# Optimization experiments

Measured on AMD Instinct MI355X. Metric: run time of the kernel, lower is better.

## Reference

```python
import jax, jax.numpy as jnp
import numpy as np

# B images, N objects/image, R relations/image; D=obj/rel feature dim, H=GGNN hidden,
# NO=num object classes, NR=num relation classes, T=GGNN time steps.
B, N, R, D, H, NO, NR, T = 8, 64, 2048, 4096, 512, 151, 51, 3


def setup_inputs() -> dict:
    key = jax.random.key(0)
    ks = jax.random.split(key, 24)
    nrm = lambda k, shp: jax.random.normal(k, shp, dtype=jnp.float32) * 0.02
    im_inds = jnp.repeat(jnp.arange(B, dtype=jnp.int32), N)          # sorted per-object image ids
    img_r = jnp.repeat(jnp.arange(B, dtype=jnp.int32), R)            # per-relation image ids
    pair = jax.random.randint(ks[0], (B * R, 2), 0, N, dtype=jnp.int32) + (img_r * N)[:, None]
    rel_inds = jnp.concatenate([img_r[:, None], pair], axis=1)        # [B*R, 3]
    return dict(
        im_inds=im_inds, rel_inds=rel_inds,
        obj_fmaps=jax.random.normal(ks[1], (B * N, D), jnp.float32),
        obj_logits=jax.random.normal(ks[2], (B * N, NO), jnp.float32),
        vr=jax.random.normal(ks[3], (B * R, D), jnp.float32),
        W_obj=nrm(ks[4], (D, H)), b_obj=jnp.zeros((H,), jnp.float32),
        W_rel=nrm(ks[5], (D, H)), b_rel=jnp.zeros((H,), jnp.float32),
        W_prob=nrm(ks[6], (NO, H)), b_prob=jnp.zeros((H,), jnp.float32),
        W_so=nrm(ks[7], (H, H)), W_oo=nrm(ks[8], (H, H)),
        W_rs=nrm(ks[9], (H, H)), W_ro=nrm(ks[10], (H, H)),
        Wz=nrm(ks[11], (H, H)), Uz=nrm(ks[12], (H, H)), bz=jnp.zeros((H,), jnp.float32),
        Wr=nrm(ks[13], (H, H)), Ur=nrm(ks[14], (H, H)), br=jnp.zeros((H,), jnp.float32),
        Wh=nrm(ks[15], (H, H)), Uh=nrm(ks[16], (H, H)), bh=jnp.zeros((H,), jnp.float32),
        W_out_rel=nrm(ks[17], (2 * H, H)), b_out_rel=jnp.zeros((H,), jnp.float32),
        W_cls_rel=nrm(ks[18], (H, NR)), b_cls_rel=jnp.zeros((NR,), jnp.float32),
        W_out_obj=nrm(ks[19], (2 * H, H)), b_out_obj=jnp.zeros((H,), jnp.float32),
        W_cls_obj=nrm(ks[20], (H, NO)), b_cls_obj=jnp.zeros((NO,), jnp.float32),
    )


def reference(im_inds, rel_inds, obj_fmaps, obj_logits, vr,
              W_obj, b_obj, W_rel, b_rel, W_prob, b_prob,
              W_so, W_oo, W_rs, W_ro,
              Wz, Uz, bz, Wr, Ur, br, Wh, Uh, bh,
              W_out_rel, b_out_rel, W_cls_rel, b_cls_rel,
              W_out_obj, b_out_obj, W_cls_obj, b_cls_obj):
    # obj_probs = softmax(obj_logits); project features + class distribution into GGNN hidden
    obj_probs = jax.nn.softmax(obj_logits, axis=-1)
    xo = (obj_fmaps @ W_obj + b_obj + obj_probs @ W_prob + b_prob).reshape(B, N, H)
    xr = (vr @ W_rel + b_rel).reshape(B, R, H)
    # per-image local indices: rel_inds[rel_s:rel_e, 1:] - obj_s
    off = (jnp.arange(B, dtype=rel_inds.dtype) * N)[:, None]
    subj = rel_inds[:, 1].reshape(B, R) - off
    objn = rel_inds[:, 2].reshape(B, R) - off

    def gru(h, m):
        z = jax.nn.sigmoid(m @ Wz + h @ Uz + bz)
        r = jax.nn.sigmoid(m @ Wr + h @ Ur + br)
        hh = jnp.tanh(m @ Wh + (r * h) @ Uh + bh)
        return (1.0 - z) * h + z * hh

    def per_image(xo_i, xr_i, s, o):
        ho, hr = xo_i, xr_i
        for _ in range(T):  # fixed recurrence depth (time_step_num)
            mr = ho[s] @ W_so + ho[o] @ W_oo                               # gather obj -> rel
            mo = (jax.ops.segment_sum(hr @ W_rs, s, num_segments=N)
                  + jax.ops.segment_sum(hr @ W_ro, o, num_segments=N))     # scatter rel -> obj
            ho, hr = gru(ho, mo), gru(hr, mr)
        rel_logits = jnp.tanh(jnp.concatenate([hr, xr_i], -1) @ W_out_rel + b_out_rel) @ W_cls_rel + b_cls_rel
        obj_ref = jnp.tanh(jnp.concatenate([ho, xo_i], -1) @ W_out_obj + b_out_obj) @ W_cls_obj + b_cls_obj
        return rel_logits, obj_ref

    rel_logits, obj_ref = jax.vmap(per_image)(xo, xr, subj, objn)
    rel_logits = rel_logits.reshape(B * R, NR)
    obj_ref = obj_ref.reshape(B * N, NO)
    scpred_softmax = jax.nn.softmax(rel_logits, axis=-1)
    scent_softmax = jax.nn.softmax(obj_ref, axis=-1)
    # sgcls, inference, no obj_labels: obj_preds = argmax over classes 1..NO-1, + 1
    obj_preds = jnp.argmax(obj_ref[:, 1:], axis=-1) + 1
    return (obj_ref, obj_preds, rel_logits, scpred_softmax, scent_softmax)
```

## Files before the change

kernel.cpp:

```cpp
#include <hip/hip_runtime.h>
#include <math.h>

#define Bn   8
#define Nn   64
#define Rn   2048
#define Dn   4096
#define Hn   512
#define NOc  151
#define NRc  51
#define Tt   3
#define BNt  (Bn*Nn)
#define BRt  (Bn*Rn)
#define Mall (BRt+BNt)

typedef __attribute__((ext_vector_type(8))) short short8;
typedef __attribute__((ext_vector_type(4))) float f32x4;

__device__ __forceinline__ float sigmf(float x){ return 1.0f/(1.0f+expf(-x)); }

__device__ __forceinline__ ushort f2bf_rne(float x){
  unsigned u = __float_as_uint(x);
  unsigned r = u + 0x7FFFu + ((u>>16)&1u);
  return (ushort)(r>>16);
}

template<int BM,int BN>
__global__ __launch_bounds__(256)
void gemm_b3(const float* __restrict__ A, const ushort* __restrict__ Bhg,
             const ushort* __restrict__ Blg, float* __restrict__ C,
             int M,int N,int K,int lda,int ldb,int ldc,
             const float* __restrict__ bias, const float* __restrict__ bias2,
             int beta,int act,int dupoff,
             int mode, const int* __restrict__ rel,
             const float* __restrict__ Gso, const float* __restrict__ G1,
             int brt, float* __restrict__ Zbuf, float* __restrict__ RHbuf,
             float* __restrict__ HXbuf)
{
  constexpr int MT = BM/32, NT = BN/32;
  __shared__ ushort Ah[BM*40], Al[BM*40], Bh[BN*40], Bl[BN*40];
  const int tid  = threadIdx.x;
  const int lane = tid & 63;
  const int wid  = tid >> 6;
  const int quad = lane >> 4, l15 = lane & 15;
  const int wm = (wid>>1)*(BM/2), wn = (wid&1)*(BN/2);
  const int bm = blockIdx.y*BM, bn = blockIdx.x*BN;

  constexpr int TPR  = 256/BM;
  constexpr int FPT  = 32/TPR;
  const int ar = tid / TPR;
  const int ak = (tid % TPR) * FPT;
  constexpr int TPRB = 256/BN;
  constexpr int SPT  = 32/TPRB;
  const int br_ = tid / TPRB;
  const int bk = (tid % TPRB) * SPT;
  const int grA = bm + ar;
  const int grB = bn + br_;
  const bool avec = ((lda&3)==0);

  f32x4 acc[MT][NT];
#pragma unroll
  for (int i=0;i<MT;i++)
#pragma unroll
    for (int j=0;j<NT;j++) acc[i][j] = (f32x4){0.f,0.f,0.f,0.f};

  float av[FPT];
  short8 bvh[SPT/8], bvl[SPT/8];

  auto load_tile = [&](int k0){
    if (grA < M && avec && k0 + ak + FPT <= K) {
      const float* p = A + (size_t)grA*lda + k0 + ak;
#pragma unroll
      for (int i=0;i<FPT/4;i++) ((float4*)av)[i] = ((const float4*)p)[i];
    } else {
#pragma unroll
      for (int i=0;i<FPT;i++){
        int gk = k0+ak+i;
        av[i] = (grA<M && gk<K) ? A[(size_t)grA*lda+gk] : 0.f;
      }
    }
    if (grB < N){
#pragma unroll
      for (int i=0;i<SPT/8;i++){
        bvh[i] = *(const short8*)(Bhg + (size_t)grB*ldb + k0 + bk + i*8);
        bvl[i] = *(const short8*)(Blg + (size_t)grB*ldb + k0 + bk + i*8);
      }
    } else {
#pragma unroll
      for (int i=0;i<SPT/8;i++){
#pragma unroll
        for (int q=0;q<8;q++){ bvh[i][q]=0; bvl[i][q]=0; }
      }
    }
  };

  load_tile(0);

  for (int k0=0; k0<K; k0+=32) {
    {
      ushort hs[FPT], ls[FPT];
#pragma unroll
      for (int i=0;i<FPT;i++){
        ushort h = f2bf_rne(av[i]);
        float hf = __uint_as_float(((unsigned)h)<<16);
        hs[i]=h; ls[i]=f2bf_rne(av[i]-hf);
      }
#pragma unroll
      for (int i=0;i<FPT;i+=8){
        short8 vh, vl;
#pragma unroll
        for (int q=0;q<8;q++){ vh[q]=(short)hs[i+q]; vl[q]=(short)ls[i+q]; }
        *(short8*)&Ah[ar*40+ak+i] = vh;
        *(short8*)&Al[ar*40+ak+i] = vl;
      }
#pragma unroll
      for (int i=0;i<SPT/8;i++){
        *(short8*)&Bh[br_*40+bk+i*8] = bvh[i];
        *(short8*)&Bl[br_*40+bk+i*8] = bvl[i];
      }
    }
    __syncthreads();
    if (k0+32 < K) load_tile(k0+32);
    {
      short8 afh[MT], afl[MT], bfh[NT], bfl[NT];
#pragma unroll
      for (int i=0;i<MT;i++){
        int o = (wm + i*16 + l15)*40 + quad*8;
        afh[i] = *(const short8*)&Ah[o];
        afl[i] = *(const short8*)&Al[o];
      }
#pragma unroll
      for (int j=0;j<NT;j++){
        int o = (wn + j*16 + l15)*40 + quad*8;
        bfh[j] = *(const short8*)&Bh[o];
        bfl[j] = *(const short8*)&Bl[o];
      }
#pragma unroll
      for (int i=0;i<MT;i++)
#pragma unroll
        for (int j=0;j<NT;j++)
          acc[i][j] = __builtin_amdgcn_mfma_f32_16x16x32_bf16(afh[i], bfh[j], acc[i][j], 0,0,0);
#pragma unroll
      for (int i=0;i<MT;i++)
#pragma unroll
        for (int j=0;j<NT;j++)
          acc[i][j] = __builtin_amdgcn_mfma_f32_16x16x32_bf16(afh[i], bfl[j], acc[i][j], 0,0,0);
#pragma unroll
      for (int i=0;i<MT;i++)
#pragma unroll
        for (int j=0;j<NT;j++)
          acc[i][j] = __builtin_amdgcn_mfma_f32_16x16x32_bf16(afl[i], bfh[j], acc[i][j], 0,0,0);
    }
    __syncthreads();
  }

  if (mode == 0) {
#pragma unroll
    for (int i=0;i<MT;i++){
      int gm0 = bm + wm + i*16 + quad*4;
#pragma unroll
      for (int j=0;j<NT;j++){
        int gn = bn + wn + j*16 + l15;
        if (gn >= N) continue;
#pragma unroll
        for (int r=0;r<4;r++){
          int gm = gm0 + r;
          if (gm >= M) continue;
          float v = acc[i][j][r];
          if (beta) v += C[(size_t)gm*ldc+gn];
          if (bias) v += bias[gn];
          if (act==1) v = sigmf(v);
          else if (act==2) v = tanhf(v);
          C[(size_t)gm*ldc+gn] = v;
          if (dupoff) C[(size_t)gm*ldc+gn+dupoff] = v;
        }
      }
    }
  } else if (mode == 1) {
#pragma unroll
    for (int i=0;i<MT;i++){
#pragma unroll
      for (int r=0;r<4;r++){
        int gm = bm + wm + i*16 + quad*4 + r;
        if (gm >= M) continue;
        bool isrel = gm < brt;
        int s=0,o=0; const float* g1row = nullptr;
        if (isrel){ s = rel[gm*3+1]; o = rel[gm*3+2]; }
        else g1row = G1 + (size_t)(gm-brt)*1536;
#pragma unroll
        for (int j=0;j<NT;j++){
          int gn = bn + wn + j*16 + l15;
          float v = acc[i][j][r];
          if (gn < 512){
            float g = isrel ? Gso[(size_t)s*3072+gn] + Gso[(size_t)o*3072+1536+gn]
                            : g1row[gn];
            Zbuf[(size_t)gm*512+gn] = sigmf(v + g + bias[gn]);
          } else {
            int h = gn - 512;
            float g = isrel ? Gso[(size_t)s*3072+512+h] + Gso[(size_t)o*3072+2048+h]
                            : g1row[512+h];
            RHbuf[(size_t)gm*512+h] = sigmf(v + g + bias2[h]) * HXbuf[(size_t)gm*1024+h];
          }
        }
      }
    }
  } else {
#pragma unroll
    for (int i=0;i<MT;i++){
#pragma unroll
      for (int r=0;r<4;r++){
        int gm = bm + wm + i*16 + quad*4 + r;
        if (gm >= M) continue;
        bool isrel = gm < brt;
        int s=0,o=0; const float* g1row = nullptr;
        if (isrel){ s = rel[gm*3+1]; o = rel[gm*3+2]; }
        else g1row = G1 + (size_t)(gm-brt)*1536;
#pragma unroll
        for (int j=0;j<NT;j++){
          int h = bn + wn + j*16 + l15;
          float v = acc[i][j][r];
          float g = isrel ? Gso[(size_t)s*3072+1024+h] + Gso[(size_t)o*3072+2560+h]
                          : g1row[1024+h];
          float hh = tanhf(v + g + bias[h]);
          float z = Zbuf[(size_t)gm*512+h];
          size_t hx = (size_t)gm*1024+h;
          HXbuf[hx] = (1.f-z)*HXbuf[hx] + z*hh;
        }
      }
    }
  }
}

__global__ __launch_bounds__(256)
void tsplit(const float* __restrict__ src,int K,int N,
            ushort* __restrict__ dh, ushort* __restrict__ dl,
            int dld,int rowoff,int koff)
{
  __shared__ float t[32][33];
  const int tx = threadIdx.x, ty = threadIdx.y;
  const int kb = blockIdx.x*32, nb = blockIdx.y*32;
#pragma unroll
  for (int r=0;r<4;r++){
    int k = kb + ty + r*8, n = nb + tx;
    t[ty+r*8][tx] = (k<K && n<N) ? src[(size_t)k*N + n] : 0.f;
  }
  __syncthreads();
#pragma unroll
  for (int r=0;r<4;r++){
    int n = nb + ty + r*8, k = kb + tx;
    if (n < N){
      float v = t[tx][ty+r*8];
      ushort h = f2bf_rne(v);
      float hf = __uint_as_float(((unsigned)h)<<16);
      ushort l = f2bf_rne(v - hf);
      size_t o = (size_t)(rowoff+n)*dld + koff + k;
      dh[o]=h; dl[o]=l;
    }
  }
}

__global__ __launch_bounds__(64)
void softmax_kernel(const float* __restrict__ in, float* __restrict__ out,
                    int cols, int ldi, int ldo, int padto)
{
  int row = blockIdx.x, lane = threadIdx.x;
  const float* rp = in + (size_t)row*ldi;
  float m = -INFINITY;
  for (int c = lane; c < cols; c += 64) m = fmaxf(m, rp[c]);
  for (int off = 32; off; off >>= 1) m = fmaxf(m, __shfl_xor(m, off));
  float s = 0.f;
  for (int c = lane; c < cols; c += 64) s += expf(rp[c]-m);
  for (int off = 32; off; off >>= 1) s += __shfl_xor(s, off);
  float inv = 1.f/s;
  float* op = out + (size_t)row*ldo;
  for (int c = lane; c < padto; c += 64)
    op[c] = (c < cols) ? expf(rp[c]-m)*inv : 0.f;
}

__global__ __launch_bounds__(64)
void argmax_kernel(const float* __restrict__ ref, float* __restrict__ preds)
{
  int row = blockIdx.x, lane = threadIdx.x;
  const float* rp = ref + (size_t)row*NOc;
  float bv = -INFINITY; int bi = NOc;
  for (int c = 1+lane; c < NOc; c += 64) { float v = rp[c]; if (v > bv) { bv=v; bi=c; } }
  for (int off=32; off; off>>=1) {
    float ov = __shfl_xor(bv, off); int oi = __shfl_xor(bi, off);
    if (ov > bv || (ov == bv && oi < bi)) { bv = ov; bi = oi; }
  }
  if (lane==0) preds[row] = (float)bi;
}

__global__ __launch_bounds__(64)
void segsum2(const float* __restrict__ HX, const int* __restrict__ rel_inds,
             float* __restrict__ SumSO)
{
  __shared__ float accS[64][64];
  __shared__ float accO[64][64];
  const int t = threadIdx.x;
  const int hb = blockIdx.x*64;
  const int img = blockIdx.z;
  const int relbase = img*Rn + blockIdx.y*(Rn/4);
  for (int ob=0; ob<64; ob++){ accS[ob][t]=0.f; accO[ob][t]=0.f; }
  for (int i=0;i<Rn/4;i++){
    int r = relbase+i;
    int s = rel_inds[r*3+1] - img*64;
    int o = rel_inds[r*3+2] - img*64;
    float v = HX[(size_t)r*1024 + hb + t];
    accS[s][t]+=v; accO[o][t]+=v;
  }
  for (int ob=0;ob<64;ob++){
    size_t rowb = (size_t)(img*64+ob)*1024 + hb + t;
    atomicAdd(&SumSO[rowb],     accS[ob][t]);
    atomicAdd(&SumSO[rowb+512], accO[ob][t]);
  }
}

#define NOFUSE 0,nullptr,nullptr,nullptr,0,nullptr,nullptr,nullptr
static void Gstd128(hipStream_t s,const float*A,const ushort*bh,const ushort*bl,float*C,
  int M,int N,int K,int lda,int ldb,int ldc,const float*bias,int beta,int act,int dupoff){
  dim3 g((N+127)/128,(M+127)/128);
  gemm_b3<128,128><<<g,256,0,s>>>(A,bh,bl,C,M,N,K,lda,ldb,ldc,bias,nullptr,beta,act,dupoff,NOFUSE);
}
static void Gstd64(hipStream_t s,const float*A,const ushort*bh,const ushort*bl,float*C,
  int M,int N,int K,int lda,int ldb,int ldc,const float*bias,int beta,int act,int dupoff){
  dim3 g((N+63)/64,(M+63)/64);
  gemm_b3<64,64><<<g,256,0,s>>>(A,bh,bl,C,M,N,K,lda,ldb,ldc,bias,nullptr,beta,act,dupoff,NOFUSE);
}
static void Gstd128x64(hipStream_t s,const float*A,const ushort*bh,const ushort*bl,float*C,
  int M,int N,int K,int lda,int ldb,int ldc,const float*bias,int beta,int act,int dupoff){
  dim3 g((N+63)/64,(M+127)/128);
  gemm_b3<128,64><<<g,256,0,s>>>(A,bh,bl,C,M,N,K,lda,ldb,ldc,bias,nullptr,beta,act,dupoff,NOFUSE);
}
static void TS(hipStream_t s,const float*src,int K,int N,ushort*dh,ushort*dl,
               int dld,int rowoff,int koff,int Kpad){
  dim3 g(Kpad/32,(N+31)/32);
  tsplit<<<g,dim3(32,8),0,s>>>(src,K,N,dh,dl,dld,rowoff,koff);
}

extern "C" void kernel_launch(void* const* d_in, const int* in_sizes, int n_in,
                              void* d_out, int out_size, void* d_ws, size_t ws_size,
                              hipStream_t stream) {
  (void)in_sizes; (void)n_in; (void)out_size; (void)ws_size;
  const int*   rel_inds   = (const int*)  d_in[1];
  const float* obj_fmaps  = (const float*)d_in[2];
  const float* obj_logits = (const float*)d_in[3];
  const float* vr         = (const float*)d_in[4];
  const float* W_obj      = (const float*)d_in[5];
  const float* b_obj      = (const float*)d_in[6];
  const float* W_rel      = (const float*)d_in[7];
  const float* b_rel      = (const float*)d_in[8];
  const float* W_prob     = (const float*)d_in[9];
  const float* b_prob     = (const float*)d_in[10];
  const float* W_so       = (const float*)d_in[11];
  const float* W_oo       = (const float*)d_in[12];
  const float* W_rs       = (const float*)d_in[13];
  const float* W_ro       = (const float*)d_in[14];
  const float* Wz         = (const float*)d_in[15];
  const float* Uz         = (const float*)d_in[16];
  const float* bz         = (const float*)d_in[17];
  const float* Wr         = (const float*)d_in[18];
  const float* Ur         = (const float*)d_in[19];
  const float* br         = (const float*)d_in[20];
  const float* Wh         = (const float*)d_in[21];
  const float* Uh         = (const float*)d_in[22];
  const float* bh         = (const float*)d_in[23];
  const float* W_out_rel  = (const float*)d_in[24];
  const float* b_out_rel  = (const float*)d_in[25];
  const float* W_cls_rel  = (const float*)d_in[26];
  const float* b_cls_rel  = (const float*)d_in[27];
  const float* W_out_obj  = (const float*)d_in[28];
  const float* b_out_obj  = (const float*)d_in[29];
  const float* W_cls_obj  = (const float*)d_in[30];
  const float* b_cls_obj  = (const float*)d_in[31];

  float* out          = (float*)d_out;
  float* out_obj_ref  = out;
  float* out_preds    = out + 77312;
  float* out_rel_log  = out + 77824;
  float* out_scpred   = out + 913408;
  float* out_scent    = out + 1748992;

  char* base = (char*)d_ws; size_t off = 0;
  auto alloc = [&](size_t bytes)->void*{ void* p = base+off; off = (off+bytes+255)&~(size_t)255; return p; };
  float*  HX    = (float*) alloc((size_t)Mall*1024*4);
  float*  Zb    = (float*) alloc((size_t)Mall*512*4);
  float*  RH    = (float*) alloc((size_t)Mall*512*4);
  ushort* Bt3h  = (ushort*)alloc((size_t)1536*512*2);
  ushort* Bt3l  = (ushort*)alloc((size_t)1536*512*2);
  ushort* BtU2h = (ushort*)alloc((size_t)1024*512*2);
  ushort* BtU2l = (ushort*)alloc((size_t)1024*512*2);
  ushort* BtUHh = (ushort*)alloc((size_t)512*512*2);
  ushort* BtUHl = (ushort*)alloc((size_t)512*512*2);
  ushort* BtPh  = (ushort*)alloc((size_t)1536*1024*2);
  ushort* BtPl  = (ushort*)alloc((size_t)1536*1024*2);
  ushort* BtORh = (ushort*)alloc((size_t)512*1024*2);
  ushort* BtORl = (ushort*)alloc((size_t)512*1024*2);
  ushort* BtCRh = (ushort*)alloc((size_t)51*512*2);
  ushort* BtCRl = (ushort*)alloc((size_t)51*512*2);
  ushort* BtOOh = (ushort*)alloc((size_t)512*1024*2);
  ushort* BtOOl = (ushort*)alloc((size_t)512*1024*2);
  ushort* BtCOh = (ushort*)alloc((size_t)151*512*2);
  ushort* BtCOl = (ushort*)alloc((size_t)151*512*2);
  ushort* BtWCh = (ushort*)alloc((size_t)3072*512*2);
  ushort* BtWCl = (ushort*)alloc((size_t)3072*512*2);
  float*  Gso   = (float*) alloc((size_t)512*3072*4);
  float*  G1    = (float*) alloc((size_t)512*1536*4);
  float*  SumSO = (float*) alloc((size_t)512*1024*4);
  float*  oprob = (float*) alloc((size_t)512*152*4);
  float*  Cobj  = (float*) alloc((size_t)512*512*4);

  ushort* BtRELh = (ushort*)Zb;
  ushort* BtRELl = BtRELh + (size_t)512*4096;
  ushort* BtOBJh = BtRELl + (size_t)512*4096;
  ushort* BtOBJl = BtOBJh + (size_t)512*4096;
  ushort* BtPRh  = BtOBJl + (size_t)512*4096;
  ushort* BtPRl  = BtPRh  + (size_t)512*160;
  float*  Wcat   = RH;
  float*  Pfp    = RH + (size_t)512*3072;

  float* HOXr = HX + (size_t)BRt*1024;

  softmax_kernel<<<512,64,0,stream>>>(obj_logits, oprob, NOc, NOc, 152, 152);
  TS(stream, W_rel,  4096,512, BtRELh,BtRELl, 4096, 0,0, 4096);
  TS(stream, W_obj,  4096,512, BtOBJh,BtOBJl, 4096, 0,0, 4096);
  TS(stream, W_prob,  151,512, BtPRh, BtPRl,   160, 0,0,  160);
  TS(stream, Wz, 512,512, Bt3h,Bt3l, 512,    0,0, 512);
  TS(stream, Wr, 512,512, Bt3h,Bt3l, 512,  512,0, 512);
  TS(stream, Wh, 512,512, Bt3h,Bt3l, 512, 1024,0, 512);
  TS(stream, Uz, 512,512, BtU2h,BtU2l, 512,   0,0, 512);
  TS(stream, Ur, 512,512, BtU2h,BtU2l, 512, 512,0, 512);
  TS(stream, Uh, 512,512, BtUHh,BtUHl, 512, 0,0, 512);
  TS(stream, W_out_rel, 1024,512, BtORh,BtORl, 1024, 0,0, 1024);
  TS(stream, W_cls_rel,  512, 51, BtCRh,BtCRl,  512, 0,0,  512);
  TS(stream, W_out_obj, 1024,512, BtOOh,BtOOl, 1024, 0,0, 1024);
  TS(stream, W_cls_obj,  512,151, BtCOh,BtCOl,  512, 0,0,  512);
  Gstd64(stream, obj_fmaps, BtOBJh,BtOBJl, HOXr+512, 512,512,4096, 4096,4096,1024, b_obj,0,0,0);
  Gstd64(stream, oprob,     BtPRh, BtPRl,  HOXr+512, 512,512, 151,  152, 160,1024, b_prob,1,0,-512);
  Gstd128(stream, vr, BtRELh,BtRELl, HX+512, BRt,512,4096, 4096,4096,1024, b_rel,0,0,-512);
  Gstd64(stream, W_so, Bt3h,Bt3l, Wcat,            512,1536,512, 512,512,3072, nullptr,0,0,0);
  Gstd64(stream, W_oo, Bt3h,Bt3l, Wcat+1536,       512,1536,512, 512,512,3072, nullptr,0,0,0);
  Gstd64(stream, W_rs, Bt3h,Bt3l, Pfp,             512,1536,512, 512,512,1536, nullptr,0,0,0);
  Gstd64(stream, W_ro, Bt3h,Bt3l, Pfp+512*1536,    512,1536,512, 512,512,1536, nullptr,0,0,0);
  TS(stream, Wcat,  512,3072, BtWCh,BtWCl,  512, 0,0,  512);
  TS(stream, Pfp,  1024,1536, BtPh, BtPl,  1024, 0,0, 1024);

  for (int t = 0; t < Tt; t++) {
    Gstd64(stream, HOXr, BtWCh,BtWCl, Gso, 512,3072,512, 1024,512,3072, nullptr,0,0,0);
    hipMemsetAsync(SumSO, 0, (size_t)512*1024*4, stream);
    segsum2<<<dim3(8,4,8),64,0,stream>>>(HX, rel_inds, SumSO);
    Gstd64(stream, SumSO, BtPh,BtPl, G1, 512,1536,1024, 1024,1024,1536, nullptr,0,0,0);
    {
      dim3 g(1024/128, Mall/128);
      gemm_b3<128,128><<<g,256,0,stream>>>(HX, BtU2h,BtU2l, nullptr,
        Mall,1024,512, 1024,512,0, bz,br,0,0,0,
        1, rel_inds, Gso, G1, BRt, Zb, RH, HX);
    }
    {
      dim3 g(512/128, Mall/128);
      gemm_b3<128,128><<<g,256,0,stream>>>(RH, BtUHh,BtUHl, nullptr,
        Mall,512,512, 512,512,0, bh,nullptr,0,0,0,
        2, rel_inds, Gso, G1, BRt, Zb, nullptr, HX);
    }
  }

  float* Crel = Zb;
  Gstd128(stream, HX, BtORh,BtORl, Crel, BRt,512,1024, 1024,1024,512, b_out_rel,0,2,0);
  Gstd128x64(stream, Crel, BtCRh,BtCRl, out_rel_log, BRt,NRc,512, 512,512,NRc, b_cls_rel,0,0,0);
  softmax_kernel<<<BRt,64,0,stream>>>(out_rel_log, out_scpred, NRc, NRc, NRc, NRc);
  Gstd64(stream, HOXr, BtOOh,BtOOl, Cobj, 512,512,1024, 1024,1024,512, b_out_obj,0,2,0);
  Gstd64(stream, Cobj, BtCOh,BtCOl, out_obj_ref, 512,NOc,512, 512,512,NOc, b_cls_obj,0,0,0);
  softmax_kernel<<<512,64,0,stream>>>(out_obj_ref, out_scent, NOc, NOc, NOc, NOc);
  argmax_kernel<<<512,64,0,stream>>>(out_obj_ref, out_preds);
}
```

Measured before the change: 2.288 ms.

## Store GEMM activations as pre-split bf16 hi/lo pairs and swizzle blocks across XCDs

GEMM epilogues now write activations (hidden state, reset-gated hidden, intermediate tanh outputs) directly as bf16 hi/lo split pairs, so downstream GEMMs load them without per-tile fp32-to-bf16 splitting. The fp32 hidden state is kept separately at width 512 for the GRU update and segment sums. Block indices are remapped so neighbouring M-tiles land on the same XCD for better L2 reuse, and the relation input GEMM moves to a 64x256 tile. The split copies double write traffic for those tensors but halve A-load bytes and remove conversion ALU work in the inner loop.

```diff
diff --git a/kernel.cpp b/kernel.cpp
--- a/kernel.cpp
+++ b/kernel.cpp
@@ -23,39 +23,53 @@
   unsigned r = u + 0x7FFFu + ((u>>16)&1u);
   return (ushort)(r>>16);
 }
-
-template<int BM,int BN>
+__device__ __forceinline__ float bf2f(ushort h){
+  return __uint_as_float(((unsigned)h)<<16);
+}
+
+template<int BM,int BN,int ASPLIT>
 __global__ __launch_bounds__(256)
-void gemm_b3(const float* __restrict__ A, const ushort* __restrict__ Bhg,
-             const ushort* __restrict__ Blg, float* __restrict__ C,
+void gemm_b3(const float* __restrict__ Af,
+             const ushort* __restrict__ Aph, const ushort* __restrict__ Apl,
+             const ushort* __restrict__ Bhg, const ushort* __restrict__ Blg,
+             float* __restrict__ Cf, const float* __restrict__ Cin,
              int M,int N,int K,int lda,int ldb,int ldc,
              const float* __restrict__ bias, const float* __restrict__ bias2,
-             int beta,int act,int dupoff,
-             int mode, const int* __restrict__ rel,
-             const float* __restrict__ Gso, const float* __restrict__ G1,
-             int brt, float* __restrict__ Zbuf, float* __restrict__ RHbuf,
-             float* __restrict__ HXbuf)
+             int act,int dupoff,
+             ushort* __restrict__ Cph, ushort* __restrict__ Cpl,int ldcp,int dupp,
+             int swz,int mode,const int* __restrict__ rel,
+             const float* __restrict__ Gso,const float* __restrict__ G1,
+             int brt,float* __restrict__ Zb,
+             ushort* __restrict__ RHh,ushort* __restrict__ RHl,
+             float* __restrict__ Hf,
+             ushort* __restrict__ HXph,ushort* __restrict__ HXpl)
 {
   constexpr int MT = BM/32, NT = BN/32;
   __shared__ ushort Ah[BM*40], Al[BM*40], Bh[BN*40], Bl[BN*40];
+
+  int bxi = blockIdx.x, byi = blockIdx.y;
+  if (swz){
+    int id  = byi*gridDim.x + bxi;
+    int mch = gridDim.y >> 3;
+    int xcd = id & 7, j = id >> 3;
+    byi = xcd*mch + j % mch;
+    bxi = j / mch;
+  }
   const int tid  = threadIdx.x;
   const int lane = tid & 63;
   const int wid  = tid >> 6;
   const int quad = lane >> 4, l15 = lane & 15;
   const int wm = (wid>>1)*(BM/2), wn = (wid&1)*(BN/2);
-  const int bm = blockIdx.y*BM, bn = blockIdx.x*BN;
-
-  constexpr int TPR  = 256/BM;
-  constexpr int FPT  = 32/TPR;
+  const int bm = byi*BM, bn = bxi*BN;
+
+  constexpr int TPR = 256/BM, CPT = 32/TPR;
   const int ar = tid / TPR;
-  const int ak = (tid % TPR) * FPT;
-  constexpr int TPRB = 256/BN;
-  constexpr int SPT  = 32/TPRB;
+  const int ak = (tid % TPR) * CPT;
+  constexpr int TPRB = 256/BN, SPT = 32/TPRB;
   const int br_ = tid / TPRB;
-  const int bk = (tid % TPRB) * SPT;
+  const int bk  = (tid % TPRB) * SPT;
   const int grA = bm + ar;
   const int grB = bn + br_;
-  const bool avec = ((lda&3)==0);
 
   f32x4 acc[MT][NT];
 #pragma unroll
@@ -63,19 +77,36 @@
 #pragma unroll
     for (int j=0;j<NT;j++) acc[i][j] = (f32x4){0.f,0.f,0.f,0.f};
 
-  float av[FPT];
+  float  avf[ASPLIT ? 1 : CPT];
+  short8 avh[ASPLIT ? CPT/8 : 1], avl[ASPLIT ? CPT/8 : 1];
   short8 bvh[SPT/8], bvl[SPT/8];
 
   auto load_tile = [&](int k0){
-    if (grA < M && avec && k0 + ak + FPT <= K) {
-      const float* p = A + (size_t)grA*lda + k0 + ak;
-#pragma unroll
-      for (int i=0;i<FPT/4;i++) ((float4*)av)[i] = ((const float4*)p)[i];
+    if constexpr (ASPLIT){
+      if (grA < M){
+#pragma unroll
+        for (int i=0;i<CPT/8;i++){
+          avh[i] = *(const short8*)(Aph + (size_t)grA*lda + k0 + ak + i*8);
+          avl[i] = *(const short8*)(Apl + (size_t)grA*lda + k0 + ak + i*8);
+        }
+      } else {
+#pragma unroll
+        for (int i=0;i<CPT/8;i++){
+#pragma unroll
+          for (int q=0;q<8;q++){ avh[i][q]=0; avl[i][q]=0; }
+        }
+      }
     } else {
-#pragma unroll
-      for (int i=0;i<FPT;i++){
-        int gk = k0+ak+i;
-        av[i] = (grA<M && gk<K) ? A[(size_t)grA*lda+gk] : 0.f;
+      if (grA < M && ((lda&3)==0) && k0 + ak + CPT <= K) {
+        const float* p = Af + (size_t)grA*lda + k0 + ak;
+#pragma unroll
+        for (int i=0;i<CPT/4;i++) ((float4*)avf)[i] = ((const float4*)p)[i];
+      } else {
+#pragma unroll
+        for (int i=0;i<CPT;i++){
+          int gk = k0+ak+i;
+          avf[i] = (grA<M && gk<K) ? Af[(size_t)grA*lda+gk] : 0.f;
+        }
       }
     }
     if (grB < N){
@@ -96,27 +127,32 @@
   load_tile(0);
 
   for (int k0=0; k0<K; k0+=32) {
-    {
-      ushort hs[FPT], ls[FPT];
-#pragma unroll
-      for (int i=0;i<FPT;i++){
-        ushort h = f2bf_rne(av[i]);
-        float hf = __uint_as_float(((unsigned)h)<<16);
-        hs[i]=h; ls[i]=f2bf_rne(av[i]-hf);
-      }
-#pragma unroll
-      for (int i=0;i<FPT;i+=8){
+    if constexpr (ASPLIT){
+#pragma unroll
+      for (int i=0;i<CPT/8;i++){
+        *(short8*)&Ah[ar*40+ak+i*8] = avh[i];
+        *(short8*)&Al[ar*40+ak+i*8] = avl[i];
+      }
+    } else {
+      ushort hs[CPT], ls[CPT];
+#pragma unroll
+      for (int i=0;i<CPT;i++){
+        ushort h = f2bf_rne(avf[i]);
+        hs[i]=h; ls[i]=f2bf_rne(avf[i]-bf2f(h));
+      }
+#pragma unroll
+      for (int i=0;i<CPT;i+=8){
         short8 vh, vl;
 #pragma unroll
         for (int q=0;q<8;q++){ vh[q]=(short)hs[i+q]; vl[q]=(short)ls[i+q]; }
         *(short8*)&Ah[ar*40+ak+i] = vh;
         *(short8*)&Al[ar*40+ak+i] = vl;
       }
-#pragma unroll
-      for (int i=0;i<SPT/8;i++){
-        *(short8*)&Bh[br_*40+bk+i*8] = bvh[i];
-        *(short8*)&Bl[br_*40+bk+i*8] = bvl[i];
-      }
+    }
+#pragma unroll
+    for (int i=0;i<SPT/8;i++){
+      *(short8*)&Bh[br_*40+bk+i*8] = bvh[i];
+      *(short8*)&Bl[br_*40+bk+i*8] = bvl[i];
     }
     __syncthreads();
     if (k0+32 < K) load_tile(k0+32);
@@ -166,12 +202,21 @@
           int gm = gm0 + r;
           if (gm >= M) continue;
           float v = acc[i][j][r];
-          if (beta) v += C[(size_t)gm*ldc+gn];
+          if (Cin)  v += Cin[(size_t)gm*ldc+gn];
           if (bias) v += bias[gn];
           if (act==1) v = sigmf(v);
           else if (act==2) v = tanhf(v);
-          C[(size_t)gm*ldc+gn] = v;
-          if (dupoff) C[(size_t)gm*ldc+gn+dupoff] = v;
+          if (Cf){
+            Cf[(size_t)gm*ldc+gn] = v;
+            if (dupoff) Cf[(size_t)gm*ldc+gn+dupoff] = v;
+          }
+          if (Cph){
+            ushort h_ = f2bf_rne(v);
+            ushort l_ = f2bf_rne(v - bf2f(h_));
+            size_t p = (size_t)gm*ldcp + gn;
+            Cph[p]=h_; Cpl[p]=l_;
+            if (dupp){ Cph[p+dupp]=h_; Cpl[p+dupp]=l_; }
+          }
         }
       }
     }
@@ -193,12 +238,15 @@
           if (gn < 512){
             float g = isrel ? Gso[(size_t)s*3072+gn] + Gso[(size_t)o*3072+1536+gn]
                             : g1row[gn];
-            Zbuf[(size_t)gm*512+gn] = sigmf(v + g + bias[gn]);
+            Zb[(size_t)gm*512+gn] = sigmf(v + g + bias[gn]);
           } else {
             int h = gn - 512;
             float g = isrel ? Gso[(size_t)s*3072+512+h] + Gso[(size_t)o*3072+2048+h]
                             : g1row[512+h];
-            RHbuf[(size_t)gm*512+h] = sigmf(v + g + bias2[h]) * HXbuf[(size_t)gm*1024+h];
+            float rhv = sigmf(v + g + bias2[h]) * Hf[(size_t)gm*512+h];
+            ushort h_ = f2bf_rne(rhv);
+            ushort l_ = f2bf_rne(rhv - bf2f(h_));
+            RHh[(size_t)gm*512+h]=h_; RHl[(size_t)gm*512+h]=l_;
           }
         }
       }
@@ -221,9 +269,14 @@
           float g = isrel ? Gso[(size_t)s*3072+1024+h] + Gso[(size_t)o*3072+2560+h]
                           : g1row[1024+h];
           float hh = tanhf(v + g + bias[h]);
-          float z = Zbuf[(size_t)gm*512+h];
-          size_t hx = (size_t)gm*1024+h;
-          HXbuf[hx] = (1.f-z)*HXbuf[hx] + z*hh;
+          size_t ix = (size_t)gm*512+h;
+          float z = Zb[ix];
+          float hn = (1.f-z)*Hf[ix] + z*hh;
+          Hf[ix] = hn;
+          ushort h_ = f2bf_rne(hn);
+          ushort l_ = f2bf_rne(hn - bf2f(h_));
+          size_t p = (size_t)gm*1024+h;
+          HXph[p]=h_; HXpl[p]=l_;
         }
       }
     }
@@ -250,8 +303,7 @@
     if (n < N){
       float v = t[tx][ty+r*8];
       ushort h = f2bf_rne(v);
-      float hf = __uint_as_float(((unsigned)h)<<16);
-      ushort l = f2bf_rne(v - hf);
+      ushort l = f2bf_rne(v - bf2f(h));
       size_t o = (size_t)(rowoff+n)*dld + koff + k;
       dh[o]=h; dl[o]=l;
     }
@@ -291,7 +343,7 @@
 }
 
 __global__ __launch_bounds__(64)
-void segsum2(const float* __restrict__ HX, const int* __restrict__ rel_inds,
+void segsum2(const float* __restrict__ Hf, const int* __restrict__ rel_inds,
              float* __restrict__ SumSO)
 {
   __shared__ float accS[64][64];
@@ -305,7 +357,7 @@
     int r = relbase+i;
     int s = rel_inds[r*3+1] - img*64;
     int o = rel_inds[r*3+2] - img*64;
-    float v = HX[(size_t)r*1024 + hb + t];
+    float v = Hf[(size_t)r*512 + hb + t];
     accS[s][t]+=v; accO[o][t]+=v;
   }
   for (int ob=0;ob<64;ob++){
@@ -315,22 +367,8 @@
   }
 }
 
-#define NOFUSE 0,nullptr,nullptr,nullptr,0,nullptr,nullptr,nullptr
-static void Gstd128(hipStream_t s,const float*A,const ushort*bh,const ushort*bl,float*C,
-  int M,int N,int K,int lda,int ldb,int ldc,const float*bias,int beta,int act,int dupoff){
-  dim3 g((N+127)/128,(M+127)/128);
-  gemm_b3<128,128><<<g,256,0,s>>>(A,bh,bl,C,M,N,K,lda,ldb,ldc,bias,nullptr,beta,act,dupoff,NOFUSE);
-}
-static void Gstd64(hipStream_t s,const float*A,const ushort*bh,const ushort*bl,float*C,
-  int M,int N,int K,int lda,int ldb,int ldc,const float*bias,int beta,int act,int dupoff){
-  dim3 g((N+63)/64,(M+63)/64);
-  gemm_b3<64,64><<<g,256,0,s>>>(A,bh,bl,C,M,N,K,lda,ldb,ldc,bias,nullptr,beta,act,dupoff,NOFUSE);
-}
-static void Gstd128x64(hipStream_t s,const float*A,const ushort*bh,const ushort*bl,float*C,
-  int M,int N,int K,int lda,int ldb,int ldc,const float*bias,int beta,int act,int dupoff){
-  dim3 g((N+63)/64,(M+127)/128);
-  gemm_b3<128,64><<<g,256,0,s>>>(A,bh,bl,C,M,N,K,lda,ldb,ldc,bias,nullptr,beta,act,dupoff,NOFUSE);
-}
+#define FZ0 0,nullptr,nullptr,nullptr,0,nullptr,nullptr,nullptr,nullptr,nullptr,nullptr
+
 static void TS(hipStream_t s,const float*src,int K,int N,ushort*dh,ushort*dl,
                int dld,int rowoff,int koff,int Kpad){
   dim3 g(Kpad/32,(N+31)/32);
@@ -382,9 +420,12 @@
 
   char* base = (char*)d_ws; size_t off = 0;
   auto alloc = [&](size_t bytes)->void*{ void* p = base+off; off = (off+bytes+255)&~(size_t)255; return p; };
-  float*  HX    = (float*) alloc((size_t)Mall*1024*4);
+  float*  Hf    = (float*) alloc((size_t)Mall*512*4);
+  ushort* HXph  = (ushort*)alloc((size_t)Mall*1024*2);
+  ushort* HXpl  = (ushort*)alloc((size_t)Mall*1024*2);
+  ushort* RHh   = (ushort*)alloc((size_t)Mall*512*2);
+  ushort* RHl   = (ushort*)alloc((size_t)Mall*512*2);
   float*  Zb    = (float*) alloc((size_t)Mall*512*4);
-  float*  RH    = (float*) alloc((size_t)Mall*512*4);
   ushort* Bt3h  = (ushort*)alloc((size_t)1536*512*2);
   ushort* Bt3l  = (ushort*)alloc((size_t)1536*512*2);
   ushort* BtU2h = (ushort*)alloc((size_t)1024*512*2);
@@ -395,19 +436,21 @@
   ushort* BtPl  = (ushort*)alloc((size_t)1536*1024*2);
   ushort* BtORh = (ushort*)alloc((size_t)512*1024*2);
   ushort* BtORl = (ushort*)alloc((size_t)512*1024*2);
-  ushort* BtCRh = (ushort*)alloc((size_t)51*512*2);
-  ushort* BtCRl = (ushort*)alloc((size_t)51*512*2);
+  ushort* BtCRh = (ushort*)alloc((size_t)64*512*2);
+  ushort* BtCRl = (ushort*)alloc((size_t)64*512*2);
   ushort* BtOOh = (ushort*)alloc((size_t)512*1024*2);
   ushort* BtOOl = (ushort*)alloc((size_t)512*1024*2);
-  ushort* BtCOh = (ushort*)alloc((size_t)151*512*2);
-  ushort* BtCOl = (ushort*)alloc((size_t)151*512*2);
+  ushort* BtCOh = (ushort*)alloc((size_t)152*512*2);
+  ushort* BtCOl = (ushort*)alloc((size_t)152*512*2);
   ushort* BtWCh = (ushort*)alloc((size_t)3072*512*2);
   ushort* BtWCl = (ushort*)alloc((size_t)3072*512*2);
   float*  Gso   = (float*) alloc((size_t)512*3072*4);
   float*  G1    = (float*) alloc((size_t)512*1536*4);
   float*  SumSO = (float*) alloc((size_t)512*1024*4);
   float*  oprob = (float*) alloc((size_t)512*152*4);
-  float*  Cobj  = (float*) alloc((size_t)512*512*4);
+  float*  Xotmp = (float*) alloc((size_t)512*512*4);
+  ushort* COph  = (ushort*)alloc((size_t)512*512*2);
+  ushort* COpl  = (ushort*)alloc((size_t)512*512*2);
 
   ushort* BtRELh = (ushort*)Zb;
   ushort* BtRELl = BtRELh + (size_t)512*4096;
@@ -415,10 +458,8 @@
   ushort* BtOBJl = BtOBJh + (size_t)512*4096;
   ushort* BtPRh  = BtOBJl + (size_t)512*4096;
   ushort* BtPRl  = BtPRh  + (size_t)512*160;
-  float*  Wcat   = RH;
-  float*  Pfp    = RH + (size_t)512*3072;
-
-  float* HOXr = HX + (size_t)BRt*1024;
+  float*  Wcat   = (float*)(BtPRl + (size_t)512*160);
+  float*  Pfp    = Wcat + (size_t)512*3072;
 
   softmax_kernel<<<512,64,0,stream>>>(obj_logits, oprob, NOc, NOc, 152, 152);
   TS(stream, W_rel,  4096,512, BtRELh,BtRELl, 4096, 0,0, 4096);
@@ -434,41 +475,92 @@
   TS(stream, W_cls_rel,  512, 51, BtCRh,BtCRl,  512, 0,0,  512);
   TS(stream, W_out_obj, 1024,512, BtOOh,BtOOl, 1024, 0,0, 1024);
   TS(stream, W_cls_obj,  512,151, BtCOh,BtCOl,  512, 0,0,  512);
-  Gstd64(stream, obj_fmaps, BtOBJh,BtOBJl, HOXr+512, 512,512,4096, 4096,4096,1024, b_obj,0,0,0);
-  Gstd64(stream, oprob,     BtPRh, BtPRl,  HOXr+512, 512,512, 151,  152, 160,1024, b_prob,1,0,-512);
-  Gstd128(stream, vr, BtRELh,BtRELl, HX+512, BRt,512,4096, 4096,4096,1024, b_rel,0,0,-512);
-  Gstd64(stream, W_so, Bt3h,Bt3l, Wcat,            512,1536,512, 512,512,3072, nullptr,0,0,0);
-  Gstd64(stream, W_oo, Bt3h,Bt3l, Wcat+1536,       512,1536,512, 512,512,3072, nullptr,0,0,0);
-  Gstd64(stream, W_rs, Bt3h,Bt3l, Pfp,             512,1536,512, 512,512,1536, nullptr,0,0,0);
-  Gstd64(stream, W_ro, Bt3h,Bt3l, Pfp+512*1536,    512,1536,512, 512,512,1536, nullptr,0,0,0);
+
+  {
+    dim3 g(8,8);
+    gemm_b3<64,64,0><<<g,256,0,stream>>>(obj_fmaps,nullptr,nullptr,BtOBJh,BtOBJl,
+      Xotmp,nullptr, 512,512,4096, 4096,4096,512, b_obj,nullptr,0,0,
+      nullptr,nullptr,0,0, 1, FZ0);
+    gemm_b3<64,64,0><<<g,256,0,stream>>>(oprob,nullptr,nullptr,BtPRh,BtPRl,
+      Hf+(size_t)BRt*512, Xotmp, 512,512,151, 152,160,512, b_prob,nullptr,0,0,
+      HXph+(size_t)BRt*1024+512, HXpl+(size_t)BRt*1024+512, 1024, -512, 1, FZ0);
+  }
+  {
+    dim3 g(2,256);
+    gemm_b3<64,256,0><<<g,256,0,stream>>>(vr,nullptr,nullptr,BtRELh,BtRELl,
+      Hf,nullptr, BRt,512,4096, 4096,4096,512, b_rel,nullptr,0,0,
+      HXph+512, HXpl+512, 1024, -512, 1, FZ0);
+  }
+  {
+    dim3 g(24,8);
+    gemm_b3<64,64,0><<<g,256,0,stream>>>(W_so,nullptr,nullptr,Bt3h,Bt3l,
+      Wcat,nullptr, 512,1536,512, 512,512,3072, nullptr,nullptr,0,0, nullptr,nullptr,0,0, 1, FZ0);
+    gemm_b3<64,64,0><<<g,256,0,stream>>>(W_oo,nullptr,nullptr,Bt3h,Bt3l,
+      Wcat+1536,nullptr, 512,1536,512, 512,512,3072, nullptr,nullptr,0,0, nullptr,nullptr,0,0, 1, FZ0);
+    gemm_b3<64,64,0><<<g,256,0,stream>>>(W_rs,nullptr,nullptr,Bt3h,Bt3l,
+      Pfp,nullptr, 512,1536,512, 512,512,1536, nullptr,nullptr,0,0, nullptr,nullptr,0,0, 1, FZ0);
+    gemm_b3<64,64,0><<<g,256,0,stream>>>(W_ro,nullptr,nullptr,Bt3h,Bt3l,
+      Pfp+(size_t)512*1536,nullptr, 512,1536,512, 512,512,1536, nullptr,nullptr,0,0, nullptr,nullptr,0,0, 1, FZ0);
+  }
   TS(stream, Wcat,  512,3072, BtWCh,BtWCl,  512, 0,0,  512);
   TS(stream, Pfp,  1024,1536, BtPh, BtPl,  1024, 0,0, 1024);
 
   for (int t = 0; t < Tt; t++) {
-    Gstd64(stream, HOXr, BtWCh,BtWCl, Gso, 512,3072,512, 1024,512,3072, nullptr,0,0,0);
+    {
+      dim3 g(48,8);
+      gemm_b3<64,64,1><<<g,256,0,stream>>>(nullptr,HXph+(size_t)BRt*1024,HXpl+(size_t)BRt*1024,
+        BtWCh,BtWCl, Gso,nullptr, 512,3072,512, 1024,512,3072,
+        nullptr,nullptr,0,0, nullptr,nullptr,0,0, 1, FZ0);
+    }
     hipMemsetAsync(SumSO, 0, (size_t)512*1024*4, stream);
-    segsum2<<<dim3(8,4,8),64,0,stream>>>(HX, rel_inds, SumSO);
-    Gstd64(stream, SumSO, BtPh,BtPl, G1, 512,1536,1024, 1024,1024,1536, nullptr,0,0,0);
+    segsum2<<<dim3(8,4,8),64,0,stream>>>(Hf, rel_inds, SumSO);
     {
-      dim3 g(1024/128, Mall/128);
-      gemm_b3<128,128><<<g,256,0,stream>>>(HX, BtU2h,BtU2l, nullptr,
-        Mall,1024,512, 1024,512,0, bz,br,0,0,0,
-        1, rel_inds, Gso, G1, BRt, Zb, RH, HX);
+      dim3 g(24,8);
+      gemm_b3<64,64,0><<<g,256,0,stream>>>(SumSO,nullptr,nullptr,BtPh,BtPl,
+        G1,nullptr, 512,1536,1024, 1024,1024,1536,
+        nullptr,nullptr,0,0, nullptr,nullptr,0,0, 1, FZ0);
     }
     {
-      dim3 g(512/128, Mall/128);
-      gemm_b3<128,128><<<g,256,0,stream>>>(RH, BtUHh,BtUHl, nullptr,
-        Mall,512,512, 512,512,0, bh,nullptr,0,0,0,
-        2, rel_inds, Gso, G1, BRt, Zb, nullptr, HX);
-    }
-  }
-
-  float* Crel = Zb;
-  Gstd128(stream, HX, BtORh,BtORl, Crel, BRt,512,1024, 1024,1024,512, b_out_rel,0,2,0);
-  Gstd128x64(stream, Crel, BtCRh,BtCRl, out_rel_log, BRt,NRc,512, 512,512,NRc, b_cls_rel,0,0,0);
+      dim3 g(8,136);
+      gemm_b3<128,128,1><<<g,256,0,stream>>>(nullptr,HXph,HXpl,BtU2h,BtU2l,
+        nullptr,nullptr, Mall,1024,512, 1024,512,0, bz,br,0,0,
+        nullptr,nullptr,0,0, 1,
+        1, rel_inds, Gso, G1, BRt, Zb, RHh,RHl, Hf, nullptr,nullptr);
+    }
+    {
+      dim3 g(4,136);
+      gemm_b3<128,128,1><<<g,256,0,stream>>>(nullptr,RHh,RHl,BtUHh,BtUHl,
+        nullptr,nullptr, Mall,512,512, 512,512,0, bh,nullptr,0,0,
+        nullptr,nullptr,0,0, 1,
+        2, rel_inds, Gso, G1, BRt, Zb, nullptr,nullptr, Hf, HXph,HXpl);
+    }
+  }
+
+  {
+    dim3 g(4,128);
+    gemm_b3<128,128,1><<<g,256,0,stream>>>(nullptr,HXph,HXpl,BtORh,BtORl,
+      nullptr,nullptr, BRt,512,1024, 1024,1024,0, b_out_rel,nullptr,2,0,
+      RHh,RHl,512,0, 1, FZ0);
+  }
+  {
+    dim3 g(1,256);
+    gemm_b3<64,64,1><<<g,256,0,stream>>>(nullptr,RHh,RHl,BtCRh,BtCRl,
+      out_rel_log,nullptr, BRt,NRc,512, 512,512,NRc, b_cls_rel,nullptr,0,0,
+      nullptr,nullptr,0,0, 1, FZ0);
+  }
   softmax_kernel<<<BRt,64,0,stream>>>(out_rel_log, out_scpred, NRc, NRc, NRc, NRc);
-  Gstd64(stream, HOXr, BtOOh,BtOOl, Cobj, 512,512,1024, 1024,1024,512, b_out_obj,0,2,0);
-  Gstd64(stream, Cobj, BtCOh,BtCOl, out_obj_ref, 512,NOc,512, 512,512,NOc, b_cls_obj,0,0,0);
+  {
+    dim3 g(8,8);
+    gemm_b3<64,64,1><<<g,256,0,stream>>>(nullptr,HXph+(size_t)BRt*1024,HXpl+(size_t)BRt*1024,
+      BtOOh,BtOOl, nullptr,nullptr, 512,512,1024, 1024,1024,0, b_out_obj,nullptr,2,0,
+      COph,COpl,512,0, 1, FZ0);
+  }
+  {
+    dim3 g(3,8);
+    gemm_b3<64,64,1><<<g,256,0,stream>>>(nullptr,COph,COpl,BtCOh,BtCOl,
+      out_obj_ref,nullptr, 512,NOc,512, 512,512,NOc, b_cls_obj,nullptr,0,0,
+      nullptr,nullptr,0,0, 1, FZ0);
+  }
   softmax_kernel<<<512,64,0,stream>>>(out_obj_ref, out_scent, NOc, NOc, NOc, NOc);
   argmax_kernel<<<512,64,0,stream>>>(out_obj_ref, out_preds);
 }
```

Measured after the change: 2.169 ms. 1.05x faster.
